# Kernel optimization log

Hardware: AMD Instinct MI355X
Metric: run time of the kernel (lower is better)

The kernel has to match this reference:

```python
import jax, jax.numpy as jnp
import numpy as np

LOG2_HASHMAP_SIZE = 19
HASHMAP_MASK = np.uint32((1 << LOG2_HASHMAP_SIZE) - 1)
# num_mf_layers=4 -> mf_layer_indices=[2,5,8,11] of the 12-level geometric
# resolution list between base=16 and finest=512
RESOLUTIONS = (30, 80, 210, 512)
PRIMES = (np.uint32(1), np.uint32(11614769), np.uint32(2654435761))
N_POINTS = 2_000_000
N_FEATS = 2

# 8 corner offsets of a 3D voxel, shape [8, 3]
CORNER_OFFSETS = jnp.array([[i, j, k] for i in (0, 1) for j in (0, 1) for k in (0, 1)], dtype=jnp.int32)


def _hash3(coords):
    # coords: [..., 3] int32 grid coordinates -> [...] int32 hash index
    c = coords.astype(jnp.uint32)
    h = (c[..., 0] * PRIMES[0]) ^ (c[..., 1] * PRIMES[1]) ^ (c[..., 2] * PRIMES[2])
    return (h & HASHMAP_MASK).astype(jnp.int32)


def setup_inputs() -> dict:
    key = jax.random.key(0)
    k1, k2 = jax.random.split(key)
    # points inside the unit bounding box
    x = jax.random.uniform(k1, (N_POINTS, 3), dtype=jnp.float32)
    # 4 hash tables, init U(-1e-4, 1e-4) as in nn.init.uniform_
    tables = jax.random.uniform(k2, (len(RESOLUTIONS), 1 << LOG2_HASHMAP_SIZE, N_FEATS),
                                minval=-1e-4, maxval=1e-4, dtype=jnp.float32)
    return {"x": x, "tables": tables}


def reference(x, tables):
    # x: [N, 3] in [0, 1]; tables: [L, 2^19, F]
    outs = []
    for li, res in enumerate(RESOLUTIONS):
        scaled = x * jnp.float32(res)          # [N, 3]
        bottom = jnp.floor(scaled)             # voxel min vertex
        t = scaled - bottom                    # relative position in voxel, [N, 3]
        corners = bottom.astype(jnp.int32)[:, None, :] + CORNER_OFFSETS[None]  # [N, 8, 3]
        idx = _hash3(corners)                  # [N, 8]
        emb = tables[li][idx]                  # gather corner embeddings, [N, 8, F]
        # trilinear weights: prod over dims of (t if offset==1 else 1-t)
        w = jnp.where(CORNER_OFFSETS[None].astype(bool), t[:, None, :], 1.0 - t[:, None, :]).prod(axis=-1)  # [N, 8]
        outs.append(jnp.einsum('nc,ncf->nf', w, emb))  # [N, F]
    return jnp.concatenate(outs, axis=-1)  # [N, L*F] = [N, 8]
```

## Files before the change

### kernel.cpp

```cpp
#include <hip/hip_runtime.h>
#include <hip/hip_fp16.h>
#include <stdint.h>

#define LOG2_HASHMAP_SIZE 19
#define HASHMAP_SIZE (1u << LOG2_HASHMAP_SIZE)
#define HASHMAP_MASK (HASHMAP_SIZE - 1u)
#define N_LEVELS 4

#define R0 31
#define DENSE0_N (R0 * R0 * R0)
#define DENSE0_BYTES (DENSE0_N * 4)

#define R1 81
#define D1_N (R1 * R1 * R1)
#define ZQ 41
#define ZP_N (2 * R1 * R1 * ZQ)
#define ZP_BYTES ((size_t)ZP_N * 8)

typedef float v4f __attribute__((ext_vector_type(4)));
typedef float v2f __attribute__((ext_vector_type(2)));

__device__ __forceinline__ uint32_t hash3(uint32_t ix, uint32_t iy, uint32_t iz) {
    return (ix ^ (iy * 11614769u) ^ (iz * 2654435761u)) & HASHMAP_MASK;
}

__device__ __forceinline__ float2 h2f(uint32_t p) {
    return __half22float2(*(const __half2*)&p);
}
__device__ __forceinline__ uint32_t f2h(float a, float b) {
    const __half2 p = __floats2half2_rn(a, b);
    return *(const uint32_t*)&p;
}

__device__ __forceinline__ float2 level_embed_p(float px, float py, float pz,
                                                const float* __restrict__ tables,
                                                int li, float r)
{
    const uint32_t P1 = 11614769u;
    const uint32_t P2 = 2654435761u;

    const float sx = px * r, sy = py * r, sz = pz * r;
    const float bx = floorf(sx), by = floorf(sy), bz = floorf(sz);
    const float tx = sx - bx, ty = sy - by, tz = sz - bz;
    const float ux = 1.0f - tx, uy = 1.0f - ty, uz = 1.0f - tz;

    const uint32_t ix = (uint32_t)(int)bx;
    const uint32_t iy = (uint32_t)(int)by;
    const uint32_t iz = (uint32_t)(int)bz;

    const uint32_t hy0 = iy * P1, hy1 = (iy + 1u) * P1;
    const uint32_t hz0 = iz * P2, hz1 = (iz + 1u) * P2;

    uint32_t S[4];
    float W[4];
    S[0] = hy0 ^ hz0;  W[0] = uy * uz;
    S[1] = hy0 ^ hz1;  W[1] = uy * tz;
    S[2] = hy1 ^ hz0;  W[2] = ty * uz;
    S[3] = hy1 ^ hz1;  W[3] = ty * tz;

    const float* tab = tables + (size_t)li * HASHMAP_SIZE * 2;
    const float2* __restrict__ tab2 = (const float2*)tab;

    float f0 = 0.0f, f1 = 0.0f;
    #pragma unroll
    for (int c = 0; c < 4; ++c) {
        const uint32_t h0 = (ix ^ S[c]) & HASHMAP_MASK;
        const uint32_t h1 = ((ix + 1u) ^ S[c]) & HASHMAP_MASK;
        const float2 e0 = tab2[h0];
        const float2 e1 = tab2[h1];
        f0 += W[c] * (ux * e0.x + tx * e1.x);
        f1 += W[c] * (ux * e0.y + tx * e1.y);
    }
    return make_float2(f0, f1);
}

__device__ __forceinline__ float2 level_embed_h16(float px, float py, float pz,
                                                  const uint32_t* __restrict__ t16,
                                                  float r)
{
    const uint32_t P1 = 11614769u;
    const uint32_t P2 = 2654435761u;

    const float sx = px * r, sy = py * r, sz = pz * r;
    const float bx = floorf(sx), by = floorf(sy), bz = floorf(sz);
    const float tx = sx - bx, ty = sy - by, tz = sz - bz;
    const float ux = 1.0f - tx, uy = 1.0f - ty, uz = 1.0f - tz;

    const uint32_t ix = (uint32_t)(int)bx;
    const uint32_t iy = (uint32_t)(int)by;
    const uint32_t iz = (uint32_t)(int)bz;

    const uint32_t hy0 = iy * P1, hy1 = (iy + 1u) * P1;
    const uint32_t hz0 = iz * P2, hz1 = (iz + 1u) * P2;

    uint32_t S[4];
    float W[4];
    S[0] = hy0 ^ hz0;  W[0] = uy * uz;
    S[1] = hy0 ^ hz1;  W[1] = uy * tz;
    S[2] = hy1 ^ hz0;  W[2] = ty * uz;
    S[3] = hy1 ^ hz1;  W[3] = ty * tz;

    float f0 = 0.0f, f1 = 0.0f;
    if ((ix & 1u) == 0u) {
        #pragma unroll
        for (int c = 0; c < 4; ++c) {
            const uint32_t h0 = (ix ^ S[c]) & HASHMAP_MASK;
            const uint2 v = ((const uint2*)t16)[h0 >> 1];
            const uint32_t p0 = (h0 & 1u) ? v.y : v.x;
            const uint32_t p1 = (h0 & 1u) ? v.x : v.y;
            const float2 e0 = h2f(p0);
            const float2 e1 = h2f(p1);
            f0 += W[c] * (ux * e0.x + tx * e1.x);
            f1 += W[c] * (ux * e0.y + tx * e1.y);
        }
    } else {
        #pragma unroll
        for (int c = 0; c < 4; ++c) {
            const uint32_t h0 = (ix ^ S[c]) & HASHMAP_MASK;
            const uint32_t h1 = ((ix + 1u) ^ S[c]) & HASHMAP_MASK;
            const float2 e0 = h2f(t16[h0]);
            const float2 e1 = h2f(t16[h1]);
            f0 += W[c] * (ux * e0.x + tx * e1.x);
            f1 += W[c] * (ux * e0.y + tx * e1.y);
        }
    }
    return make_float2(f0, f1);
}

__global__ __launch_bounds__(256) void convert_fp16(
    const float* __restrict__ tables, uint32_t* __restrict__ t16)
{
    const int i = blockIdx.x * blockDim.x + threadIdx.x;
    if (i >= 2 * (int)HASHMAP_SIZE) return;
    const float2 e = ((const float2*)tables)[2 * HASHMAP_SIZE + i];
    t16[i] = f2h(e.x, e.y);
}

__global__ __launch_bounds__(256) void build_dense0(
    const float* __restrict__ tables, uint32_t* __restrict__ dense0)
{
    const int v = blockIdx.x * blockDim.x + threadIdx.x;
    if (v >= DENSE0_N) return;
    const int vx = v / (R0 * R0);
    const int rem = v - vx * (R0 * R0);
    const int vy = rem / R0;
    const int vz = rem - vy * R0;
    const uint32_t h = hash3((uint32_t)vx, (uint32_t)vy, (uint32_t)vz);
    const float2 e = ((const float2*)tables)[h];
    dense0[v] = f2h(e.x, e.y);
}

__global__ __launch_bounds__(256) void build_dense1(
    const float* __restrict__ tables, uint32_t* __restrict__ d1)
{
    const int v = blockIdx.x * blockDim.x + threadIdx.x;
    if (v >= D1_N) return;
    const int vx = v / (R1 * R1);
    const int rem = v - vx * (R1 * R1);
    const int vy = rem / R1;
    const int vz = rem - vy * R1;
    const uint32_t h = hash3((uint32_t)vx, (uint32_t)vy, (uint32_t)vz);
    const float2 e = ((const float2*)tables)[HASHMAP_SIZE + h];
    d1[v] = f2h(e.x, e.y);
}

__global__ __launch_bounds__(256) void expand_zpair(
    const uint32_t* __restrict__ d1, uint2* __restrict__ zp)
{
    const int t = blockIdx.x * blockDim.x + threadIdx.x;
    if (t >= ZP_N) return;
    const int per_copy = R1 * R1 * ZQ;
    const int p = t / per_copy;
    int rem = t - p * per_copy;
    const int vx = rem / (R1 * ZQ);
    rem -= vx * (R1 * ZQ);
    const int vy = rem / ZQ;
    const int zq = rem - vy * ZQ;
    int z0 = 2 * zq + p;
    int z1 = z0 + 1;
    z0 = min(z0, R1 - 1);
    z1 = min(z1, R1 - 1);
    const uint32_t* base = d1 + ((size_t)vx * R1 + vy) * R1;
    uint2 q;
    q.x = base[z0];
    q.y = base[z1];
    zp[t] = q;
}

__global__ __launch_bounds__(256) void pass1_zpair(
    const float* __restrict__ x, const uint2* __restrict__ zp,
    uint32_t* __restrict__ ws, int n)
{
    const int i = blockIdx.x * blockDim.x + threadIdx.x;
    if (i >= n) return;
    const float px = __builtin_nontemporal_load(x + 3 * (size_t)i + 0);
    const float py = __builtin_nontemporal_load(x + 3 * (size_t)i + 1);
    const float pz = __builtin_nontemporal_load(x + 3 * (size_t)i + 2);

    const float sx = px * 80.0f, sy = py * 80.0f, sz = pz * 80.0f;
    const float bx = floorf(sx), by = floorf(sy), bz = floorf(sz);
    const float tx = sx - bx, ty = sy - by, tz = sz - bz;
    const float ux = 1.0f - tx, uy = 1.0f - ty, uz = 1.0f - tz;
    const int ix = (int)bx, iy = (int)by, iz = (int)bz;

    const int p  = iz & 1;
    const int zq = iz >> 1;
    const size_t base00 = (((size_t)p * R1 + ix) * R1 + iy) * ZQ + zq;
    const uint2 q00 = zp[base00];
    const uint2 q01 = zp[base00 + ZQ];
    const uint2 q10 = zp[base00 + (size_t)R1 * ZQ];
    const uint2 q11 = zp[base00 + (size_t)R1 * ZQ + ZQ];

    const float2 a00 = h2f(q00.x), a00z = h2f(q00.y);
    const float2 a01 = h2f(q01.x), a01z = h2f(q01.y);
    const float2 a10 = h2f(q10.x), a10z = h2f(q10.y);
    const float2 a11 = h2f(q11.x), a11z = h2f(q11.y);

    const float w00 = ux * uy, w01 = ux * ty, w10 = tx * uy, w11 = tx * ty;
    const float f0 = w00 * (uz * a00.x + tz * a00z.x)
                   + w01 * (uz * a01.x + tz * a01z.x)
                   + w10 * (uz * a10.x + tz * a10z.x)
                   + w11 * (uz * a11.x + tz * a11z.x);
    const float f1 = w00 * (uz * a00.y + tz * a00z.y)
                   + w01 * (uz * a01.y + tz * a01z.y)
                   + w10 * (uz * a10.y + tz * a10z.y)
                   + w11 * (uz * a11.y + tz * a11z.y);

    __builtin_nontemporal_store(f2h(f0, f1), ws + i);
}

__global__ __launch_bounds__(256) void pass2_hash(
    const float* __restrict__ x, const uint32_t* __restrict__ t16,
    uint32_t* __restrict__ ws, int n)
{
    const int i = blockIdx.x * blockDim.x + threadIdx.x;
    if (i >= n) return;
    const float px = __builtin_nontemporal_load(x + 3 * (size_t)i + 0);
    const float py = __builtin_nontemporal_load(x + 3 * (size_t)i + 1);
    const float pz = __builtin_nontemporal_load(x + 3 * (size_t)i + 2);
    const float2 e = level_embed_h16(px, py, pz, t16, 210.0f);
    __builtin_nontemporal_store(f2h(e.x, e.y), ws + i);
}

extern __shared__ uint32_t s_dense[];

__global__ __launch_bounds__(1024) void final16_kernel(
    const float* __restrict__ x, const uint32_t* __restrict__ t16_l3,
    const uint32_t* __restrict__ dense0,
    const uint32_t* __restrict__ ws1, const uint32_t* __restrict__ ws2,
    float* __restrict__ out, int n)
{
    for (int i = threadIdx.x; i < DENSE0_N; i += 1024)
        s_dense[i] = dense0[i];
    __syncthreads();

    const size_t stride = (size_t)gridDim.x * 1024;
    for (size_t i = (size_t)blockIdx.x * 1024 + threadIdx.x; i < (size_t)n; i += stride) {
        const float px = __builtin_nontemporal_load(x + 3 * i + 0);
        const float py = __builtin_nontemporal_load(x + 3 * i + 1);
        const float pz = __builtin_nontemporal_load(x + 3 * i + 2);

        const float2 e3 = level_embed_h16(px, py, pz, t16_l3, 512.0f);

        const float sx = px * 30.0f, sy = py * 30.0f, sz = pz * 30.0f;
        const float bx = floorf(sx), by = floorf(sy), bz = floorf(sz);
        const float tx = sx - bx, ty = sy - by, tz = sz - bz;
        const float uxv = 1.0f - tx, uyv = 1.0f - ty, uzv = 1.0f - tz;
        const int ix = (int)bx, iy = (int)by, iz = (int)bz;
        const int lin = (ix * R0 + iy) * R0 + iz;

        float f0 = 0.0f, f1 = 0.0f;
        #pragma unroll
        for (int dx = 0; dx < 2; ++dx) {
            const float wx = dx ? tx : uxv;
            #pragma unroll
            for (int dy = 0; dy < 2; ++dy) {
                const float wxy = wx * (dy ? ty : uyv);
                const int base = lin + (dx * R0 + dy) * R0;
                const float2 c0 = h2f(s_dense[base]);
                const float2 c1 = h2f(s_dense[base + 1]);
                f0 += wxy * (uzv * c0.x + tz * c1.x);
                f1 += wxy * (uzv * c0.y + tz * c1.y);
            }
        }

        const float2 e1 = h2f(__builtin_nontemporal_load(ws1 + i));
        const float2 e2 = h2f(__builtin_nontemporal_load(ws2 + i));

        v4f* op = (v4f*)(out + 8 * i);
        v4f lo = {f0, f1, e1.x, e1.y};
        v4f hi = {e2.x, e2.y, e3.x, e3.y};
        __builtin_nontemporal_store(lo, op);
        __builtin_nontemporal_store(hi, op + 1);
    }
}

__global__ __launch_bounds__(256) void pass_direct_kernel(
    const float* __restrict__ x, const float* __restrict__ tables,
    float* __restrict__ out, int li, float r, int n)
{
    const int i = blockIdx.x * blockDim.x + threadIdx.x;
    if (i >= n) return;
    const float px = x[3 * (size_t)i + 0];
    const float py = x[3 * (size_t)i + 1];
    const float pz = x[3 * (size_t)i + 2];
    const float2 e = level_embed_p(px, py, pz, tables, li, r);
    float2* op = (float2*)(out + 8 * (size_t)i + 2 * li);
    *op = e;
}

extern "C" void kernel_launch(void* const* d_in, const int* in_sizes, int n_in,
                              void* d_out, int out_size, void* d_ws, size_t ws_size,
                              hipStream_t stream) {
    const float* x = (const float*)d_in[0];
    const float* tables = (const float*)d_in[1];
    float* out = (float*)d_out;
    const int n = in_sizes[0] / 3;

    const size_t t16_bytes = 2 * (size_t)HASHMAP_SIZE * 4;
    const size_t off_zp    = t16_bytes;
    const size_t off_d1    = off_zp + ZP_BYTES;
    const size_t off_d0    = off_d1 + (size_t)D1_N * 4;
    const size_t off_ws1   = off_d0 + DENSE0_BYTES;
    const size_t off_ws2   = off_ws1 + (size_t)n * 4;
    const size_t ws_needed = off_ws2 + (size_t)n * 4;

    bool fused_ok = (ws_size >= ws_needed);
    if (fused_ok) {
        static int attr_ok = -1;
        if (attr_ok < 0) {
            attr_ok = (hipFuncSetAttribute(
                           reinterpret_cast<const void*>(final16_kernel),
                           hipFuncAttributeMaxDynamicSharedMemorySize,
                           DENSE0_BYTES) == hipSuccess) ? 1 : 0;
        }
        fused_ok = (attr_ok == 1);
    }

    if (fused_ok) {
        char* wsb = (char*)d_ws;
        uint32_t* t16    = (uint32_t*)wsb;
        uint2*    zp     = (uint2*)(wsb + off_zp);
        uint32_t* d1     = (uint32_t*)(wsb + off_d1);
        uint32_t* dense0 = (uint32_t*)(wsb + off_d0);
        uint32_t* ws1    = (uint32_t*)(wsb + off_ws1);
        uint32_t* ws2    = (uint32_t*)(wsb + off_ws2);

        convert_fp16<<<(2 * HASHMAP_SIZE + 255) / 256, 256, 0, stream>>>(tables, t16);
        build_dense0<<<(DENSE0_N + 255) / 256, 256, 0, stream>>>(tables, dense0);
        build_dense1<<<(D1_N + 255) / 256, 256, 0, stream>>>(tables, d1);
        expand_zpair<<<(ZP_N + 255) / 256, 256, 0, stream>>>(d1, zp);

        const int block = 256;
        const int grid = (n + block - 1) / block;
        pass1_zpair<<<grid, block, 0, stream>>>(x, zp, ws1, n);
        pass2_hash<<<grid, block, 0, stream>>>(x, t16, ws2, n);
        final16_kernel<<<256, 1024, DENSE0_BYTES, stream>>>(
            x, t16 + HASHMAP_SIZE, dense0, ws1, ws2, out, n);
    } else {
        const float res[N_LEVELS] = {30.0f, 80.0f, 210.0f, 512.0f};
        const int block = 256;
        const int grid = (n + block - 1) / block;
        for (int li = 0; li < N_LEVELS; ++li) {
            pass_direct_kernel<<<grid, block, 0, stream>>>(
                x, tables, out, li, res[li], n);
        }
    }
}
```

Baseline: 257.0 us.

## Reorder level-1 z-pair table to x,zq,y layout with 16-byte vector loads

The duplicated even/odd z-pair table for level 1 becomes a single copy laid out as [x][zq][y], so adjacent y rows sit next to each other. Each lookup then fetches two neighbouring y entries with one 16-byte load per x slice: two loads for even z and four for odd z, instead of four 8-byte loads. This halves the precomputed table size and its build cost and widens the memory transactions. In exchange, odd-z points need extra loads and a data-dependent branch, and the 16-byte loads may be only 8-byte aligned.

```diff
diff --git a/kernel.cpp b/kernel.cpp
--- a/kernel.cpp
+++ b/kernel.cpp
@@ -12,13 +12,12 @@
 #define DENSE0_BYTES (DENSE0_N * 4)
 
 #define R1 81
+#define ZQ1 41
 #define D1_N (R1 * R1 * R1)
-#define ZQ 41
-#define ZP_N (2 * R1 * R1 * ZQ)
+#define ZP_N (R1 * ZQ1 * R1)
 #define ZP_BYTES ((size_t)ZP_N * 8)
 
 typedef float v4f __attribute__((ext_vector_type(4)));
-typedef float v2f __attribute__((ext_vector_type(2)));
 
 __device__ __forceinline__ uint32_t hash3(uint32_t ix, uint32_t iy, uint32_t iz) {
     return (ix ^ (iy * 11614769u) ^ (iz * 2654435761u)) & HASHMAP_MASK;
@@ -30,6 +29,12 @@
 __device__ __forceinline__ uint32_t f2h(float a, float b) {
     const __half2 p = __floats2half2_rn(a, b);
     return *(const uint32_t*)&p;
+}
+
+__device__ __forceinline__ uint4 load16u(const uint2* p) {
+    uint4 v;
+    __builtin_memcpy(&v, p, 16);
+    return v;
 }
 
 __device__ __forceinline__ float2 level_embed_p(float px, float py, float pz,
@@ -164,30 +169,25 @@
     d1[v] = f2h(e.x, e.y);
 }
 
-__global__ __launch_bounds__(256) void expand_zpair(
+__global__ __launch_bounds__(256) void expand_zp(
     const uint32_t* __restrict__ d1, uint2* __restrict__ zp)
 {
     const int t = blockIdx.x * blockDim.x + threadIdx.x;
     if (t >= ZP_N) return;
-    const int per_copy = R1 * R1 * ZQ;
-    const int p = t / per_copy;
-    int rem = t - p * per_copy;
-    const int vx = rem / (R1 * ZQ);
-    rem -= vx * (R1 * ZQ);
-    const int vy = rem / ZQ;
-    const int zq = rem - vy * ZQ;
-    int z0 = 2 * zq + p;
-    int z1 = z0 + 1;
-    z0 = min(z0, R1 - 1);
-    z1 = min(z1, R1 - 1);
-    const uint32_t* base = d1 + ((size_t)vx * R1 + vy) * R1;
+    const int x  = t / (ZQ1 * R1);
+    int rem = t - x * (ZQ1 * R1);
+    const int zq = rem / R1;
+    const int y  = rem - zq * R1;
+    const int z0 = 2 * zq;
+    const int z1 = min(z0 + 1, R1 - 1);
+    const uint32_t* base = d1 + ((size_t)x * R1 + y) * R1;
     uint2 q;
     q.x = base[z0];
     q.y = base[z1];
     zp[t] = q;
 }
 
-__global__ __launch_bounds__(256) void pass1_zpair(
+__global__ __launch_bounds__(256) void pass1_zp(
     const float* __restrict__ x, const uint2* __restrict__ zp,
     uint32_t* __restrict__ ws, int n)
 {
@@ -203,28 +203,35 @@
     const float ux = 1.0f - tx, uy = 1.0f - ty, uz = 1.0f - tz;
     const int ix = (int)bx, iy = (int)by, iz = (int)bz;
 
-    const int p  = iz & 1;
     const int zq = iz >> 1;
-    const size_t base00 = (((size_t)p * R1 + ix) * R1 + iy) * ZQ + zq;
-    const uint2 q00 = zp[base00];
-    const uint2 q01 = zp[base00 + ZQ];
-    const uint2 q10 = zp[base00 + (size_t)R1 * ZQ];
-    const uint2 q11 = zp[base00 + (size_t)R1 * ZQ + ZQ];
-
-    const float2 a00 = h2f(q00.x), a00z = h2f(q00.y);
-    const float2 a01 = h2f(q01.x), a01z = h2f(q01.y);
-    const float2 a10 = h2f(q10.x), a10z = h2f(q10.y);
-    const float2 a11 = h2f(q11.x), a11z = h2f(q11.y);
-
-    const float w00 = ux * uy, w01 = ux * ty, w10 = tx * uy, w11 = tx * ty;
-    const float f0 = w00 * (uz * a00.x + tz * a00z.x)
-                   + w01 * (uz * a01.x + tz * a01z.x)
-                   + w10 * (uz * a10.x + tz * a10z.x)
-                   + w11 * (uz * a11.x + tz * a11z.x);
-    const float f1 = w00 * (uz * a00.y + tz * a00z.y)
-                   + w01 * (uz * a01.y + tz * a01z.y)
-                   + w10 * (uz * a10.y + tz * a10z.y)
-                   + w11 * (uz * a11.y + tz * a11z.y);
+    const size_t rowx0 = ((size_t)ix * ZQ1 + zq) * R1 + iy;
+    const size_t rowx1 = rowx0 + (size_t)ZQ1 * R1;
+
+    float2 a00, a01, a10, a11;
+    float2 b00, b01, b10, b11;
+    if ((iz & 1) == 0) {
+        const uint4 a = load16u(zp + rowx0);
+        const uint4 b = load16u(zp + rowx1);
+        a00 = h2f(a.x); a01 = h2f(a.y); a10 = h2f(a.z); a11 = h2f(a.w);
+        b00 = h2f(b.x); b01 = h2f(b.y); b10 = h2f(b.z); b11 = h2f(b.w);
+    } else {
+        const uint4 a0 = load16u(zp + rowx0);
+        const uint4 a1 = load16u(zp + rowx0 + R1);
+        const uint4 b0 = load16u(zp + rowx1);
+        const uint4 b1 = load16u(zp + rowx1 + R1);
+        a00 = h2f(a0.y); a01 = h2f(a1.x); a10 = h2f(a0.w); a11 = h2f(a1.z);
+        b00 = h2f(b0.y); b01 = h2f(b1.x); b10 = h2f(b0.w); b11 = h2f(b1.z);
+    }
+
+    const float w00 = ux * uy, w10 = ux * ty, wx0 = tx * uy, wx1 = tx * ty;
+    const float f0 = w00 * (uz * a00.x + tz * a01.x)
+                   + w10 * (uz * a10.x + tz * a11.x)
+                   + wx0 * (uz * b00.x + tz * b01.x)
+                   + wx1 * (uz * b10.x + tz * b11.x);
+    const float f1 = w00 * (uz * a00.y + tz * a01.y)
+                   + w10 * (uz * a10.y + tz * a11.y)
+                   + wx0 * (uz * b00.y + tz * b01.y)
+                   + wx1 * (uz * b10.y + tz * b11.y);
 
     __builtin_nontemporal_store(f2h(f0, f1), ws + i);
 }
@@ -349,11 +356,11 @@
         convert_fp16<<<(2 * HASHMAP_SIZE + 255) / 256, 256, 0, stream>>>(tables, t16);
         build_dense0<<<(DENSE0_N + 255) / 256, 256, 0, stream>>>(tables, dense0);
         build_dense1<<<(D1_N + 255) / 256, 256, 0, stream>>>(tables, d1);
-        expand_zpair<<<(ZP_N + 255) / 256, 256, 0, stream>>>(d1, zp);
+        expand_zp<<<(ZP_N + 255) / 256, 256, 0, stream>>>(d1, zp);
 
         const int block = 256;
         const int grid = (n + block - 1) / block;
-        pass1_zpair<<<grid, block, 0, stream>>>(x, zp, ws1, n);
+        pass1_zp<<<grid, block, 0, stream>>>(x, zp, ws1, n);
         pass2_hash<<<grid, block, 0, stream>>>(x, t16, ws2, n);
         final16_kernel<<<256, 1024, DENSE0_BYTES, stream>>>(
             x, t16 + HASHMAP_SIZE, dense0, ws1, ws2, out, n);
```

Result: faster. 247.6 us (-3.7%).
